# Kernel optimization log

Measured on AMD Instinct MI355X. Metric: run time of the kernel, lower is better.

The kernel has to match this reference:

```python
import jax, jax.numpy as jnp
import numpy as np

D_MODEL = 512
N_PAIRS = D_MODEL // 2
B, T = 8, 4096


def setup_inputs() -> dict:
    key = jax.random.key(0)
    ks = jax.random.split(key, 7)
    scale = 1.0 / np.sqrt(D_MODEL)
    return {
        "x_seq": jax.random.normal(ks[0], (B, T, D_MODEL), dtype=jnp.float32),
        "W_angle": jax.random.uniform(ks[1], (D_MODEL, N_PAIRS), jnp.float32, -scale, scale),
        "b_angle": jnp.zeros((N_PAIRS,), jnp.float32),
        "W_decay": jax.random.uniform(ks[2], (D_MODEL, 1), jnp.float32, -scale, scale),
        "b_decay": jnp.full((1,), 1.4, jnp.float32),
        "W_input": jax.random.uniform(ks[3], (D_MODEL, D_MODEL), jnp.float32, -scale, scale),
        "b_input": jax.random.uniform(ks[4], (D_MODEL,), jnp.float32, -scale, scale),
    }


def _givens_ssm(x_seq, W_angle, b_angle, W_decay, b_decay, W_input, b_input):
    Bb, Tt, D = x_seq.shape
    P = D // 2
    angles = jnp.einsum("btd,dp->btp", x_seq, W_angle) + b_angle          # [B,T,P]
    decays = jax.nn.sigmoid(jnp.einsum("btd,dk->btk", x_seq, W_decay) + b_decay)[..., 0]  # [B,T]
    inj = jnp.einsum("btd,de->bte", x_seq, W_input) + b_input              # [B,T,D]
    inj = inj.reshape(Bb, Tt, P, 2)

    # scan over time: h_t = decay_t * Rot(angles_t) h_{t-1} + inj_t, pairwise 2x2 rotations
    def step(h, inp):
        a, d, u = inp  # a:[B,P], d:[B], u:[B,P,2]
        c, s = jnp.cos(a), jnp.sin(a)
        he = c * h[..., 0] - s * h[..., 1]
        ho = s * h[..., 0] + c * h[..., 1]
        h_new = d[:, None, None] * jnp.stack([he, ho], axis=-1) + u
        return h_new, h_new

    h0 = jnp.zeros((Bb, P, 2), x_seq.dtype)
    xs = (jnp.swapaxes(angles, 0, 1), jnp.swapaxes(decays, 0, 1), jnp.swapaxes(inj, 0, 1))
    _, states = jax.lax.scan(step, h0, xs)  # [T,B,P,2]
    return jnp.swapaxes(states, 0, 1).reshape(Bb, Tt, D)


def reference(x_seq, W_angle, b_angle, W_decay, b_decay, W_input, b_input):
    return _givens_ssm(x_seq, W_angle, b_angle, W_decay, b_decay, W_input, b_input)
```

## Files before the change

kernel.cpp:

```cpp
#include <hip/hip_runtime.h>
#include <math.h>

typedef _Float16 half_t;
typedef __attribute__((ext_vector_type(8))) _Float16 half8;
typedef __attribute__((ext_vector_type(4))) _Float16 half4;
typedef __attribute__((ext_vector_type(4))) float floatx4;

#define BATCH   8
#define SEQ     4096
#define DM      512
#define NP      256
#define M_TOT   32768
#define NTOT    768
#define CHUNKS  128
#define CHUNK_LEN 32

__device__ __forceinline__ void async_load16(const void* g, void* l) {
    __builtin_amdgcn_global_load_lds((const __attribute__((address_space(1))) void*)g,
                                     (__attribute__((address_space(3))) void*)l,
                                     16, 0, 0);
}

__global__ __launch_bounds__(256) void decay_convert(const float* __restrict__ X,
                                                     const float* __restrict__ Wd,
                                                     const float* __restrict__ bd,
                                                     float* __restrict__ dec,
                                                     half_t* __restrict__ Xh) {
    const int wave = threadIdx.x >> 6;
    const int lane = threadIdx.x & 63;
    const int row  = blockIdx.x * 4 + wave;
    const float4* xr = (const float4*)(X + (size_t)row * DM);
    const float4* wd = (const float4*)Wd;
    float sum = 0.0f;
#pragma unroll
    for (int i = 0; i < 2; ++i) {
        const int c = lane + i * 64;
        float4 v = xr[c];
        float4 w = wd[c];
        sum += v.x * w.x + v.y * w.y + v.z * w.z + v.w * w.w;
        half4 h = {(half_t)v.x, (half_t)v.y, (half_t)v.z, (half_t)v.w};
        *(half4*)(Xh + (size_t)row * DM + c * 4) = h;
    }
#pragma unroll
    for (int off = 32; off > 0; off >>= 1) sum += __shfl_down(sum, off, 64);
    if (lane == 0) {
        float z = sum + bd[0];
        dec[row] = 1.0f / (1.0f + __expf(-z));
    }
}

__global__ __launch_bounds__(256) void wcat_transpose(const float* __restrict__ Wi,
                                                      const float* __restrict__ Wa,
                                                      half_t* __restrict__ Wt) {
    const int idx = blockIdx.x * 256 + threadIdx.x;
    const int n = idx >> 9;
    const int k = idx & 511;
    float v = (n < DM) ? Wi[(size_t)k * DM + n] : Wa[(size_t)k * NP + (n - DM)];
    Wt[idx] = (half_t)v;
}

__global__ __launch_bounds__(256) void gemm_fused(const half_t* __restrict__ Xh,
                                                  const half_t* __restrict__ Wt,
                                                  const float* __restrict__ bi,
                                                  const float* __restrict__ ba,
                                                  float* __restrict__ out,
                                                  half_t* __restrict__ angles) {
    __shared__ __align__(16) char As[8192];
    __shared__ __align__(16) char Bs[8192];

    const int bm   = blockIdx.x;
    const int bn   = blockIdx.y;
    const int tid  = threadIdx.x;
    const int wave = tid >> 6;
    const int lane = tid & 63;
    const int quad = lane >> 4;
    const int l16  = lane & 15;
    const int wrow = wave >> 1;
    const int wcol = wave & 1;

    floatx4 acc[4][4];
#pragma unroll
    for (int i = 0; i < 4; ++i)
#pragma unroll
        for (int j = 0; j < 4; ++j) acc[i][j] = (floatx4){0.f, 0.f, 0.f, 0.f};

    const int s0 = wave * 128 + lane;
    const int s1 = s0 + 64;
    const int r0 = s0 >> 2, kql0 = (s0 & 3) ^ ((r0 >> 1) & 3);
    const int r1 = s1 >> 2, kql1 = (s1 & 3) ^ ((r1 >> 1) & 3);
    const half_t* gA0 = Xh + (size_t)(bm * 128 + r0) * DM + kql0 * 8;
    const half_t* gA1 = Xh + (size_t)(bm * 128 + r1) * DM + kql1 * 8;
    const half_t* gB0 = Wt + (size_t)(bn * 128 + r0) * DM + kql0 * 8;
    const half_t* gB1 = Wt + (size_t)(bn * 128 + r1) * DM + kql1 * 8;
    char* lA0 = As + wave * 2048;
    char* lA1 = As + wave * 2048 + 1024;
    char* lB0 = Bs + wave * 2048;
    char* lB1 = Bs + wave * 2048 + 1024;

    for (int k0 = 0; k0 < DM; k0 += 32) {
        async_load16(gA0 + k0, lA0);
        async_load16(gA1 + k0, lA1);
        async_load16(gB0 + k0, lB0);
        async_load16(gB1 + k0, lB1);
        __syncthreads();

        half8 af[4], bf[4];
#pragma unroll
        for (int mt = 0; mt < 4; ++mt) {
            const int r = wrow * 64 + mt * 16 + l16;
            af[mt] = *(const half8*)(As + r * 64 + ((quad ^ ((r >> 1) & 3)) << 4));
        }
#pragma unroll
        for (int nt = 0; nt < 4; ++nt) {
            const int r = wcol * 64 + nt * 16 + l16;
            bf[nt] = *(const half8*)(Bs + r * 64 + ((quad ^ ((r >> 1) & 3)) << 4));
        }
#pragma unroll
        for (int mt = 0; mt < 4; ++mt)
#pragma unroll
            for (int nt = 0; nt < 4; ++nt)
                acc[mt][nt] = __builtin_amdgcn_mfma_f32_16x16x32_f16(af[mt], bf[nt],
                                                                     acc[mt][nt], 0, 0, 0);
        __syncthreads();
    }

    const int colbase = bn * 128 + wcol * 64;
#pragma unroll
    for (int nt = 0; nt < 4; ++nt) {
        const int col = colbase + nt * 16 + l16;
        const bool is_inj = col < DM;
        const float bias = is_inj ? bi[col] : ba[col - DM];
#pragma unroll
        for (int mt = 0; mt < 4; ++mt) {
            const int rowb = bm * 128 + wrow * 64 + mt * 16 + quad * 4;
#pragma unroll
            for (int r = 0; r < 4; ++r) {
                const float v = acc[mt][nt][r] + bias;
                const int row = rowb + r;
                if (is_inj) out[(size_t)row * DM + col] = v;
                else        angles[(size_t)row * NP + (col - DM)] = (half_t)v;
            }
        }
    }
}

__global__ __launch_bounds__(256) void scan_phase1(const half_t* __restrict__ angles,
                                                   const float* __restrict__ decays,
                                                   float* __restrict__ out,
                                                   float* __restrict__ thetaC,
                                                   float2* __restrict__ hend,
                                                   float* __restrict__ Dprod) {
    const int b = blockIdx.x / CHUNKS;
    const int c = blockIdx.x % CHUNKS;
    const int p = threadIdx.x;
    const int t0 = c * CHUNK_LEN;
    float2* out2 = (float2*)out;

    float h0 = 0.0f, h1 = 0.0f, th = 0.0f, dc = 1.0f;
#pragma unroll 4
    for (int i = 0; i < CHUNK_LEN; ++i) {
        const int t = t0 + i;
        const size_t idx = (size_t)(b * SEQ + t) * NP + p;
        float a = (float)angles[idx];
        float d = decays[b * SEQ + t];
        float2 u = out2[idx];
        float s, cc;
        __sincosf(a, &s, &cc);
        float he = cc * h0 - s * h1;
        float ho = s * h0 + cc * h1;
        h0 = fmaf(d, he, u.x);
        h1 = fmaf(d, ho, u.y);
        out2[idx] = make_float2(h0, h1);
        th += a;
        dc *= d;
    }
    const size_t cidx = (size_t)(b * CHUNKS + c) * NP + p;
    thetaC[cidx] = th;
    hend[cidx]   = make_float2(h0, h1);
    if (p == 0) Dprod[b * CHUNKS + c] = dc;
}

__global__ __launch_bounds__(256) void scan_chunks(const float* __restrict__ thetaC,
                                                   const float2* __restrict__ hend,
                                                   const float* __restrict__ Dprod,
                                                   float2* __restrict__ hentry) {
    const int b = blockIdx.x;
    const int p = threadIdx.x;
    float h0 = 0.0f, h1 = 0.0f;
    for (int c = 0; c < CHUNKS; ++c) {
        const size_t cidx = (size_t)(b * CHUNKS + c) * NP + p;
        hentry[cidx] = make_float2(h0, h1);
        float th = thetaC[cidx];
        float D  = Dprod[b * CHUNKS + c];
        float2 he = hend[cidx];
        float s, cc;
        __sincosf(th, &s, &cc);
        float n0 = fmaf(D, cc * h0 - s * h1, he.x);
        float n1 = fmaf(D, s * h0 + cc * h1, he.y);
        h0 = n0;
        h1 = n1;
    }
}

__global__ __launch_bounds__(256) void scan_fixup(const half_t* __restrict__ angles,
                                                  const float* __restrict__ decays,
                                                  const float2* __restrict__ hentry,
                                                  float* __restrict__ out) {
    const int b = blockIdx.x / CHUNKS;
    const int c = blockIdx.x % CHUNKS;
    if (c == 0) return;
    const int p = threadIdx.x;
    const int t0 = c * CHUNK_LEN;
    float2* out2 = (float2*)out;

    float2 v = hentry[(size_t)(b * CHUNKS + c) * NP + p];
#pragma unroll 4
    for (int i = 0; i < CHUNK_LEN; ++i) {
        const int t = t0 + i;
        const size_t idx = (size_t)(b * SEQ + t) * NP + p;
        float a = (float)angles[idx];
        float d = decays[b * SEQ + t];
        float s, cc;
        __sincosf(a, &s, &cc);
        float n0 = d * (cc * v.x - s * v.y);
        float n1 = d * (s * v.x + cc * v.y);
        v = make_float2(n0, n1);
        float2 o = out2[idx];
        o.x += v.x;
        o.y += v.y;
        out2[idx] = o;
    }
}

extern "C" void kernel_launch(void* const* d_in, const int* in_sizes, int n_in,
                              void* d_out, int out_size, void* d_ws, size_t ws_size,
                              hipStream_t stream) {
    const float* x  = (const float*)d_in[0];
    const float* Wa = (const float*)d_in[1];
    const float* ba = (const float*)d_in[2];
    const float* Wd = (const float*)d_in[3];
    const float* bd = (const float*)d_in[4];
    const float* Wi = (const float*)d_in[5];
    const float* bi = (const float*)d_in[6];
    float* out = (float*)d_out;

    char* ws = (char*)d_ws;
    half_t* x_h     = (half_t*)(ws);
    float*  thetaC  = (float*)(ws);
    float2* hend    = (float2*)(ws + 1048576);
    float*  Dprod   = (float*)(ws + 3145728);
    float2* hentry  = (float2*)(ws + 3149824);
    half_t* angles  = (half_t*)(ws + 33554432);
    float*  decays  = (float*)(ws + 50331648);
    half_t* Wcat_t  = (half_t*)(ws + 50462720);

    decay_convert<<<M_TOT / 4, 256, 0, stream>>>(x, Wd, bd, decays, x_h);
    wcat_transpose<<<(NTOT * DM) / 256, 256, 0, stream>>>(Wi, Wa, Wcat_t);
    gemm_fused<<<dim3(M_TOT / 128, NTOT / 128), 256, 0, stream>>>(x_h, Wcat_t, bi, ba, out, angles);

    scan_phase1<<<BATCH * CHUNKS, 256, 0, stream>>>(angles, decays, out, thetaC, hend, Dprod);
    scan_chunks<<<BATCH, 256, 0, stream>>>(thetaC, hend, Dprod, hentry);
    scan_fixup<<<BATCH * CHUNKS, 256, 0, stream>>>(angles, decays, hentry, out);
}
```

Measured before the change: 232.4 us.

## Store injection in fp16 and recompute scan in final pass instead of fixup

The GEMM now writes the injection term as fp16 to a workspace buffer instead of fp32 into the output. Phase one becomes a read-only summary pass, and the final pass recomputes the full recurrence from the chunk entry state, writing the output once. This avoids the read-modify-write of the fp32 output. Other changes: chunks are halved to 16 steps, each thread handles two pairs with vector loads, decay_convert does two rows per wave, the weight transpose goes through shared memory, and the chunk scan is split across 32 blocks. Storing injection in fp16 loses precision, and the serial chunk scan now runs over twice as many chunks.

```diff
diff --git a/kernel.cpp b/kernel.cpp
--- a/kernel.cpp
+++ b/kernel.cpp
@@ -4,6 +4,7 @@
 typedef _Float16 half_t;
 typedef __attribute__((ext_vector_type(8))) _Float16 half8;
 typedef __attribute__((ext_vector_type(4))) _Float16 half4;
+typedef __attribute__((ext_vector_type(2))) _Float16 half2v;
 typedef __attribute__((ext_vector_type(4))) float floatx4;
 
 #define BATCH   8
@@ -12,8 +13,8 @@
 #define NP      256
 #define M_TOT   32768
 #define NTOT    768
-#define CHUNKS  128
-#define CHUNK_LEN 32
+#define CHUNKS  256
+#define CHUNK_LEN 16
 
 __device__ __forceinline__ void async_load16(const void* g, void* l) {
     __builtin_amdgcn_global_load_lds((const __attribute__((address_space(1))) void*)g,
@@ -28,42 +29,65 @@
                                                      half_t* __restrict__ Xh) {
     const int wave = threadIdx.x >> 6;
     const int lane = threadIdx.x & 63;
-    const int row  = blockIdx.x * 4 + wave;
-    const float4* xr = (const float4*)(X + (size_t)row * DM);
+    const int row0 = blockIdx.x * 8 + wave * 2;
+    const float4* x0 = (const float4*)(X + (size_t)row0 * DM);
+    const float4* x1 = x0 + 128;
     const float4* wd = (const float4*)Wd;
-    float sum = 0.0f;
-#pragma unroll
-    for (int i = 0; i < 2; ++i) {
-        const int c = lane + i * 64;
-        float4 v = xr[c];
-        float4 w = wd[c];
-        sum += v.x * w.x + v.y * w.y + v.z * w.z + v.w * w.w;
-        half4 h = {(half_t)v.x, (half_t)v.y, (half_t)v.z, (half_t)v.w};
-        *(half4*)(Xh + (size_t)row * DM + c * 4) = h;
-    }
-#pragma unroll
-    for (int off = 32; off > 0; off >>= 1) sum += __shfl_down(sum, off, 64);
+    float4 a0 = x0[2 * lane], a1 = x0[2 * lane + 1];
+    float4 b0 = x1[2 * lane], b1 = x1[2 * lane + 1];
+    float4 w0 = wd[2 * lane], w1 = wd[2 * lane + 1];
+    float s0 = a0.x * w0.x + a0.y * w0.y + a0.z * w0.z + a0.w * w0.w
+             + a1.x * w1.x + a1.y * w1.y + a1.z * w1.z + a1.w * w1.w;
+    float s1 = b0.x * w0.x + b0.y * w0.y + b0.z * w0.z + b0.w * w0.w
+             + b1.x * w1.x + b1.y * w1.y + b1.z * w1.z + b1.w * w1.w;
+    half8 h0 = {(half_t)a0.x, (half_t)a0.y, (half_t)a0.z, (half_t)a0.w,
+                (half_t)a1.x, (half_t)a1.y, (half_t)a1.z, (half_t)a1.w};
+    half8 h1 = {(half_t)b0.x, (half_t)b0.y, (half_t)b0.z, (half_t)b0.w,
+                (half_t)b1.x, (half_t)b1.y, (half_t)b1.z, (half_t)b1.w};
+    *(half8*)(Xh + (size_t)row0 * DM + lane * 8) = h0;
+    *(half8*)(Xh + (size_t)(row0 + 1) * DM + lane * 8) = h1;
+#pragma unroll
+    for (int off = 32; off > 0; off >>= 1) {
+        s0 += __shfl_down(s0, off, 64);
+        s1 += __shfl_down(s1, off, 64);
+    }
     if (lane == 0) {
-        float z = sum + bd[0];
-        dec[row] = 1.0f / (1.0f + __expf(-z));
+        dec[row0]     = 1.0f / (1.0f + __expf(-(s0 + bd[0])));
+        dec[row0 + 1] = 1.0f / (1.0f + __expf(-(s1 + bd[0])));
     }
 }
 
 __global__ __launch_bounds__(256) void wcat_transpose(const float* __restrict__ Wi,
                                                       const float* __restrict__ Wa,
                                                       half_t* __restrict__ Wt) {
-    const int idx = blockIdx.x * 256 + threadIdx.x;
-    const int n = idx >> 9;
-    const int k = idx & 511;
-    float v = (n < DM) ? Wi[(size_t)k * DM + n] : Wa[(size_t)k * NP + (n - DM)];
-    Wt[idx] = (half_t)v;
+    __shared__ float tile[64][65];
+    const int bn_ = blockIdx.x >> 3;
+    const int bk_ = blockIdx.x & 7;
+    const int n0 = bn_ * 64, k0 = bk_ * 64;
+    const int c = threadIdx.x & 63;
+    const int r = threadIdx.x >> 6;
+    const bool from_wi = (n0 < DM);
+    const float* src = from_wi ? Wi : Wa;
+    const int ncols   = from_wi ? DM : NP;
+    const int ncol0   = from_wi ? n0 : (n0 - DM);
+#pragma unroll
+    for (int i = 0; i < 16; ++i) {
+        const int rr = r + i * 4;
+        tile[rr][c] = src[(size_t)(k0 + rr) * ncols + ncol0 + c];
+    }
+    __syncthreads();
+#pragma unroll
+    for (int i = 0; i < 16; ++i) {
+        const int rr = r + i * 4;
+        Wt[(size_t)(n0 + rr) * DM + k0 + c] = (half_t)tile[c][rr];
+    }
 }
 
 __global__ __launch_bounds__(256) void gemm_fused(const half_t* __restrict__ Xh,
                                                   const half_t* __restrict__ Wt,
                                                   const float* __restrict__ bi,
                                                   const float* __restrict__ ba,
-                                                  float* __restrict__ out,
+                                                  half_t* __restrict__ injh,
                                                   half_t* __restrict__ angles) {
     __shared__ __align__(16) char As[8192];
     __shared__ __align__(16) char Bs[8192];
@@ -137,62 +161,69 @@
             for (int r = 0; r < 4; ++r) {
                 const float v = acc[mt][nt][r] + bias;
                 const int row = rowb + r;
-                if (is_inj) out[(size_t)row * DM + col] = v;
+                if (is_inj) injh[(size_t)row * DM + col] = (half_t)v;
                 else        angles[(size_t)row * NP + (col - DM)] = (half_t)v;
             }
         }
     }
 }
 
-__global__ __launch_bounds__(256) void scan_phase1(const half_t* __restrict__ angles,
-                                                   const float* __restrict__ decays,
-                                                   float* __restrict__ out,
-                                                   float* __restrict__ thetaC,
-                                                   float2* __restrict__ hend,
-                                                   float* __restrict__ Dprod) {
-    const int b = blockIdx.x / CHUNKS;
-    const int c = blockIdx.x % CHUNKS;
-    const int p = threadIdx.x;
-    const int t0 = c * CHUNK_LEN;
-    float2* out2 = (float2*)out;
-
-    float h0 = 0.0f, h1 = 0.0f, th = 0.0f, dc = 1.0f;
+__global__ __launch_bounds__(256) void scan_sum1(const half_t* __restrict__ angles,
+                                                 const float* __restrict__ decays,
+                                                 const half_t* __restrict__ injh,
+                                                 float* __restrict__ thetaC,
+                                                 float2* __restrict__ hend,
+                                                 float* __restrict__ Dprod) {
+    const int b   = blockIdx.x >> 7;
+    const int sub = threadIdx.x >> 7;
+    const int th  = threadIdx.x & 127;
+    const int c   = (blockIdx.x & 127) * 2 + sub;
+    const int p0  = th * 2;
+    const int t0  = c * CHUNK_LEN;
+
+    const half_t* ap = angles + (size_t)(b * SEQ + t0) * NP + p0;
+    const half_t* ip = injh + (size_t)(b * SEQ + t0) * DM + 2 * p0;
+    const float*  dp = decays + b * SEQ + t0;
+
+    float h0a = 0, h1a = 0, h0b = 0, h1b = 0, tha = 0, thb = 0, dc = 1.0f;
 #pragma unroll 4
     for (int i = 0; i < CHUNK_LEN; ++i) {
-        const int t = t0 + i;
-        const size_t idx = (size_t)(b * SEQ + t) * NP + p;
-        float a = (float)angles[idx];
-        float d = decays[b * SEQ + t];
-        float2 u = out2[idx];
-        float s, cc;
-        __sincosf(a, &s, &cc);
-        float he = cc * h0 - s * h1;
-        float ho = s * h0 + cc * h1;
-        h0 = fmaf(d, he, u.x);
-        h1 = fmaf(d, ho, u.y);
-        out2[idx] = make_float2(h0, h1);
-        th += a;
-        dc *= d;
-    }
-    const size_t cidx = (size_t)(b * CHUNKS + c) * NP + p;
-    thetaC[cidx] = th;
-    hend[cidx]   = make_float2(h0, h1);
-    if (p == 0) Dprod[b * CHUNKS + c] = dc;
-}
-
-__global__ __launch_bounds__(256) void scan_chunks(const float* __restrict__ thetaC,
-                                                   const float2* __restrict__ hend,
-                                                   const float* __restrict__ Dprod,
-                                                   float2* __restrict__ hentry) {
-    const int b = blockIdx.x;
-    const int p = threadIdx.x;
-    float h0 = 0.0f, h1 = 0.0f;
+        half2v av = *(const half2v*)(ap + (size_t)i * NP);
+        half4  uv = *(const half4*)(ip + (size_t)i * DM);
+        float d = dp[i];
+        float a0 = (float)av[0], a1 = (float)av[1];
+        float s0, c0, s1, c1;
+        __sincosf(a0, &s0, &c0);
+        __sincosf(a1, &s1, &c1);
+        float n0a = fmaf(d, c0 * h0a - s0 * h1a, (float)uv[0]);
+        float n1a = fmaf(d, s0 * h0a + c0 * h1a, (float)uv[1]);
+        float n0b = fmaf(d, c1 * h0b - s1 * h1b, (float)uv[2]);
+        float n1b = fmaf(d, s1 * h0b + c1 * h1b, (float)uv[3]);
+        h0a = n0a; h1a = n1a; h0b = n0b; h1b = n1b;
+        tha += a0; thb += a1; dc *= d;
+    }
+    const size_t cbase = (size_t)(b * CHUNKS + c) * NP + p0;
+    *(float2*)(thetaC + cbase) = make_float2(tha, thb);
+    hend[cbase]     = make_float2(h0a, h1a);
+    hend[cbase + 1] = make_float2(h0b, h1b);
+    if (th == 0) Dprod[b * CHUNKS + c] = dc;
+}
+
+__global__ __launch_bounds__(64) void scan_chunks(const float* __restrict__ thetaC,
+                                                  const float2* __restrict__ hend,
+                                                  const float* __restrict__ Dprod,
+                                                  float2* __restrict__ hentry) {
+    const int b = blockIdx.x >> 2;
+    const int p = (blockIdx.x & 3) * 64 + threadIdx.x;
+    const float* Dp = Dprod + b * CHUNKS;
+    float h0 = 0, h1 = 0;
+#pragma unroll 4
     for (int c = 0; c < CHUNKS; ++c) {
-        const size_t cidx = (size_t)(b * CHUNKS + c) * NP + p;
-        hentry[cidx] = make_float2(h0, h1);
-        float th = thetaC[cidx];
-        float D  = Dprod[b * CHUNKS + c];
-        float2 he = hend[cidx];
+        const size_t idx = (size_t)(b * CHUNKS + c) * NP + p;
+        hentry[idx] = make_float2(h0, h1);
+        float th = thetaC[idx];
+        float D  = Dp[c];
+        float2 he = hend[idx];
         float s, cc;
         __sincosf(th, &s, &cc);
         float n0 = fmaf(D, cc * h0 - s * h1, he.x);
@@ -202,33 +233,43 @@
     }
 }
 
-__global__ __launch_bounds__(256) void scan_fixup(const half_t* __restrict__ angles,
+__global__ __launch_bounds__(256) void scan_final(const half_t* __restrict__ angles,
                                                   const float* __restrict__ decays,
+                                                  const half_t* __restrict__ injh,
                                                   const float2* __restrict__ hentry,
                                                   float* __restrict__ out) {
-    const int b = blockIdx.x / CHUNKS;
-    const int c = blockIdx.x % CHUNKS;
-    if (c == 0) return;
-    const int p = threadIdx.x;
-    const int t0 = c * CHUNK_LEN;
-    float2* out2 = (float2*)out;
-
-    float2 v = hentry[(size_t)(b * CHUNKS + c) * NP + p];
+    const int b   = blockIdx.x >> 7;
+    const int sub = threadIdx.x >> 7;
+    const int th  = threadIdx.x & 127;
+    const int c   = (blockIdx.x & 127) * 2 + sub;
+    const int p0  = th * 2;
+    const int t0  = c * CHUNK_LEN;
+
+    const half_t* ap = angles + (size_t)(b * SEQ + t0) * NP + p0;
+    const half_t* ip = injh + (size_t)(b * SEQ + t0) * DM + 2 * p0;
+    const float*  dp = decays + b * SEQ + t0;
+    float*        op = out + (size_t)(b * SEQ + t0) * DM + 2 * p0;
+
+    const size_t ebase = (size_t)(b * CHUNKS + c) * NP + p0;
+    float2 ea = hentry[ebase];
+    float2 eb = hentry[ebase + 1];
+    float h0a = ea.x, h1a = ea.y, h0b = eb.x, h1b = eb.y;
+
 #pragma unroll 4
     for (int i = 0; i < CHUNK_LEN; ++i) {
-        const int t = t0 + i;
-        const size_t idx = (size_t)(b * SEQ + t) * NP + p;
-        float a = (float)angles[idx];
-        float d = decays[b * SEQ + t];
-        float s, cc;
-        __sincosf(a, &s, &cc);
-        float n0 = d * (cc * v.x - s * v.y);
-        float n1 = d * (s * v.x + cc * v.y);
-        v = make_float2(n0, n1);
-        float2 o = out2[idx];
-        o.x += v.x;
-        o.y += v.y;
-        out2[idx] = o;
+        half2v av = *(const half2v*)(ap + (size_t)i * NP);
+        half4  uv = *(const half4*)(ip + (size_t)i * DM);
+        float d = dp[i];
+        float a0 = (float)av[0], a1 = (float)av[1];
+        float s0, c0, s1, c1;
+        __sincosf(a0, &s0, &c0);
+        __sincosf(a1, &s1, &c1);
+        float n0a = fmaf(d, c0 * h0a - s0 * h1a, (float)uv[0]);
+        float n1a = fmaf(d, s0 * h0a + c0 * h1a, (float)uv[1]);
+        float n0b = fmaf(d, c1 * h0b - s1 * h1b, (float)uv[2]);
+        float n1b = fmaf(d, s1 * h0b + c1 * h1b, (float)uv[3]);
+        h0a = n0a; h1a = n1a; h0b = n0b; h1b = n1b;
+        *(float4*)(op + (size_t)i * DM) = make_float4(h0a, h1a, h0b, h1b);
     }
 }
 
@@ -247,18 +288,19 @@
     char* ws = (char*)d_ws;
     half_t* x_h     = (half_t*)(ws);
     float*  thetaC  = (float*)(ws);
-    float2* hend    = (float2*)(ws + 1048576);
-    float*  Dprod   = (float*)(ws + 3145728);
-    float2* hentry  = (float2*)(ws + 3149824);
+    float2* hend    = (float2*)(ws + 2097152);
+    float*  Dprod   = (float*)(ws + 6291456);
+    float2* hentry  = (float2*)(ws + 6299648);
     half_t* angles  = (half_t*)(ws + 33554432);
-    float*  decays  = (float*)(ws + 50331648);
-    half_t* Wcat_t  = (half_t*)(ws + 50462720);
-
-    decay_convert<<<M_TOT / 4, 256, 0, stream>>>(x, Wd, bd, decays, x_h);
-    wcat_transpose<<<(NTOT * DM) / 256, 256, 0, stream>>>(Wi, Wa, Wcat_t);
-    gemm_fused<<<dim3(M_TOT / 128, NTOT / 128), 256, 0, stream>>>(x_h, Wcat_t, bi, ba, out, angles);
-
-    scan_phase1<<<BATCH * CHUNKS, 256, 0, stream>>>(angles, decays, out, thetaC, hend, Dprod);
-    scan_chunks<<<BATCH, 256, 0, stream>>>(thetaC, hend, Dprod, hentry);
-    scan_fixup<<<BATCH * CHUNKS, 256, 0, stream>>>(angles, decays, hentry, out);
-}
+    half_t* injh    = (half_t*)(ws + 50331648);
+    float*  decays  = (float*)(ws + 83886080);
+    half_t* Wcat_t  = (half_t*)(ws + 84017152);
+
+    decay_convert<<<M_TOT / 8, 256, 0, stream>>>(x, Wd, bd, decays, x_h);
+    wcat_transpose<<<96, 256, 0, stream>>>(Wi, Wa, Wcat_t);
+    gemm_fused<<<dim3(M_TOT / 128, NTOT / 128), 256, 0, stream>>>(x_h, Wcat_t, bi, ba, injh, angles);
+
+    scan_sum1<<<BATCH * CHUNKS / 2, 256, 0, stream>>>(angles, decays, injh, thetaC, hend, Dprod);
+    scan_chunks<<<32, 64, 0, stream>>>(thetaC, hend, Dprod, hentry);
+    scan_final<<<BATCH * CHUNKS / 2, 256, 0, stream>>>(angles, decays, injh, hentry, out);
+}
```

Result: no change. 233.5 us (+0.5%).
